# Kernel optimization log

Hardware: AMD Instinct MI355X
Metric: run time of the kernel (lower is better)

## Reference

```python
import jax, jax.numpy as jnp
import numpy as np

NUM_HEADS = 16


def setup_inputs() -> dict:
    key = jax.random.key(0)
    ks = jax.random.split(key, 8)
    B_, N, C = 2048, 64, 512
    nW = 64
    return {
        "x": jax.random.normal(ks[0], (B_, N, C), dtype=jnp.float32),
        "pe": jax.random.normal(ks[1], (1, N, C), dtype=jnp.float32),
        "rpe": jax.random.normal(ks[2], (NUM_HEADS, N, N), dtype=jnp.float32),
        "mask": jax.random.normal(ks[3], (nW, N, N), dtype=jnp.float32),
        "qkv_w": jax.random.normal(ks[4], (3 * C, C), dtype=jnp.float32) * 0.02,
        "qkv_b": jax.random.normal(ks[5], (3 * C,), dtype=jnp.float32) * 0.02,
        "proj_w": jax.random.normal(ks[6], (C, C), dtype=jnp.float32) * 0.02,
        "proj_b": jax.random.normal(ks[7], (C,), dtype=jnp.float32) * 0.02,
    }


def reference(x, pe, rpe, mask, qkv_w, qkv_b, proj_w, proj_b):
    B_, N, C = x.shape
    H = NUM_HEADS
    hd = C // H
    scale = hd ** -0.5
    xp = x + pe  # (B_, N, C)
    qkv = xp @ qkv_w.T + qkv_b  # (B_, N, 3C)
    qkv = qkv.reshape(B_, N, 3, H, hd).transpose(2, 0, 3, 1, 4)  # (3, B_, H, N, hd)
    q, k, v = qkv[0], qkv[1], qkv[2]
    attn = jnp.einsum("bhnd,bhmd->bhnm", q * scale, k)  # (B_, H, N, N)
    attn = attn + rpe[None]  # broadcast rpe over batch
    nW = mask.shape[0]
    attn = attn.reshape(B_ // nW, nW, H, N, N) + mask[None, :, None]
    attn = attn.reshape(B_, H, N, N)
    attn = jax.nn.softmax(attn, axis=-1)
    out = jnp.einsum("bhnm,bhmd->bhnd", attn, v)  # (B_, H, N, hd)
    out = out.transpose(0, 2, 1, 3).reshape(B_, N, C)
    return out @ proj_w.T + proj_b
```

## Files before the change

### kernel.cpp

```cpp
#include <hip/hip_runtime.h>
#include <hip/hip_bf16.h>
#include <cstdint>

typedef __bf16 bf16;
typedef __bf16 bf16x8_t __attribute__((ext_vector_type(8)));
typedef __bf16 bf16x4_t __attribute__((ext_vector_type(4)));
typedef float  f32x4_t  __attribute__((ext_vector_type(4)));

#define MFMA16(a, b, c) __builtin_amdgcn_mfma_f32_16x16x32_bf16((a), (b), (c), 0, 0, 0)

__device__ __forceinline__ void gload_lds16(const bf16* g, bf16* l) {
    __builtin_amdgcn_global_load_lds(
        (const __attribute__((address_space(1))) void*)g,
        (__attribute__((address_space(3))) void*)l,
        16, 0, 0);
}

__global__ void k_wprep(const float* __restrict__ wq, const float* __restrict__ wp,
                        bf16* __restrict__ wqb, bf16* __restrict__ wpb) {
    int t = blockIdx.x * 256 + threadIdx.x;
    int stride = gridDim.x * 256;
    for (int i = t; i < 196608; i += stride) {
        float4 v = ((const float4*)wq)[i];
        bf16x4_t o; o[0]=(bf16)v.x; o[1]=(bf16)v.y; o[2]=(bf16)v.z; o[3]=(bf16)v.w;
        ((bf16x4_t*)wqb)[i] = o;
    }
    for (int i = t; i < 65536; i += stride) {
        float4 v = ((const float4*)wp)[i];
        bf16x4_t o; o[0]=(bf16)v.x; o[1]=(bf16)v.y; o[2]=(bf16)v.z; o[3]=(bf16)v.w;
        ((bf16x4_t*)wpb)[i] = o;
    }
}

__global__ __launch_bounds__(512, 4) void k_qkv_attn(
    const float* __restrict__ x,
    const float* __restrict__ pe,
    const float* __restrict__ rpe,
    const float* __restrict__ mask,
    const float* __restrict__ qkv_b,
    const bf16*  __restrict__ wq,
    bf16* __restrict__ ao)
{
    __shared__ bf16 Ws[96 * 128];
    __shared__ bf16 qs[2][64 * 40];
    __shared__ bf16 ks[2][64 * 40];
    __shared__ bf16 vts[2][32 * 72];
    __shared__ bf16 ps[2][64 * 72];

    const int tid  = threadIdx.x;
    const int lane = tid & 63;
    const int wave = tid >> 6;
    const int win  = wave >> 2;
    const int lr   = lane & 15;
    const int lg   = lane >> 4;
    const int row0 = (wave & 3) * 16;
    const int b2   = blockIdx.x * 2 + win;
    const int wi   = b2 & 63;

    bf16x8_t a[16];
    {
        const float* xr = x  + ((size_t)(b2 * 64 + row0 + lr)) * 512;
        const float* pr = pe + (size_t)(row0 + lr) * 512;
#pragma unroll
        for (int kc = 0; kc < 16; ++kc) {
            int k = kc * 32 + lg * 8;
            float4 x0 = *(const float4*)(xr + k);
            float4 x1 = *(const float4*)(xr + k + 4);
            float4 p0 = *(const float4*)(pr + k);
            float4 p1 = *(const float4*)(pr + k + 4);
            bf16x8_t v;
            v[0]=(bf16)(x0.x+p0.x); v[1]=(bf16)(x0.y+p0.y);
            v[2]=(bf16)(x0.z+p0.z); v[3]=(bf16)(x0.w+p0.w);
            v[4]=(bf16)(x1.x+p1.x); v[5]=(bf16)(x1.y+p1.y);
            v[6]=(bf16)(x1.z+p1.z); v[7]=(bf16)(x1.w+p1.w);
            a[kc] = v;
        }
    }

    const float SCALE = 0.17677669529663687f;

    for (int h = 0; h < 16; ++h) {
        f32x4_t acc[6] = {};
#pragma unroll
        for (int kt = 0; kt < 4; ++kt) {
#pragma unroll
            for (int ii = 0; ii < 3; ++ii) {
                int instr = wave * 3 + ii;
                int r  = instr * 4 + (lane >> 4);
                int s  = lane & 15;
                int gp = (s & 8) | ((s & 7) ^ (r & 7));
                int R  = ((r >> 5) << 9) + (h << 5) + (r & 31);
                gload_lds16(wq + (size_t)R * 512 + kt * 128 + gp * 8,
                            &Ws[instr * 512]);
            }
            __syncthreads();
#pragma unroll
            for (int k2 = 0; k2 < 4; ++k2) {
                const int kc = kt * 4 + k2;
#pragma unroll
                for (int j = 0; j < 6; ++j) {
                    int row  = j * 16 + lr;
                    int p    = k2 * 4 + lg;
                    int phys = (p & 8) | ((p & 7) ^ (row & 7));
                    bf16x8_t bfrag = *(const bf16x8_t*)&Ws[row * 128 + phys * 8];
                    acc[j] = MFMA16(a[kc], bfrag, acc[j]);
                }
            }
            __syncthreads();
        }

#pragma unroll
        for (int j = 0; j < 6; ++j) {
            int which = j >> 1;
            int colh  = (j & 1) * 16 + lr;
            float bj = qkv_b[which * 512 + h * 32 + colh];
#pragma unroll
            for (int r = 0; r < 4; ++r) {
                int row = row0 + lg * 4 + r;
                float val = acc[j][r] + bj;
                if (which == 0)      qs[win][row * 40 + colh] = (bf16)val;
                else if (which == 1) ks[win][row * 40 + colh] = (bf16)val;
                else                 vts[win][colh * 72 + row] = (bf16)val;
            }
        }
        __syncthreads();

        const float* rp = rpe  + ((size_t)h)  * 4096;
        const float* mp = mask + ((size_t)wi) * 4096;
        float rm[4][4];
#pragma unroll
        for (int j = 0; j < 4; ++j) {
            int col = j * 16 + lr;
#pragma unroll
            for (int r = 0; r < 4; ++r) {
                int row = row0 + lg * 4 + r;
                rm[j][r] = rp[row * 64 + col] + mp[row * 64 + col];
            }
        }

        bf16x8_t aq = *(const bf16x8_t*)&qs[win][(row0 + lr) * 40 + lg * 8];
        f32x4_t s[4];
        f32x4_t zero = {};
#pragma unroll
        for (int j = 0; j < 4; ++j) {
            bf16x8_t bk = *(const bf16x8_t*)&ks[win][(j * 16 + lr) * 40 + lg * 8];
            s[j] = MFMA16(aq, bk, zero);
        }

        float mx[4] = {-1e30f, -1e30f, -1e30f, -1e30f};
#pragma unroll
        for (int j = 0; j < 4; ++j)
#pragma unroll
            for (int r = 0; r < 4; ++r) {
                float t = s[j][r] * SCALE + rm[j][r];
                s[j][r] = t;
                mx[r] = fmaxf(mx[r], t);
            }
#pragma unroll
        for (int r = 0; r < 4; ++r) {
            float m = mx[r];
            m = fmaxf(m, __shfl_xor(m, 1));
            m = fmaxf(m, __shfl_xor(m, 2));
            m = fmaxf(m, __shfl_xor(m, 4));
            m = fmaxf(m, __shfl_xor(m, 8));
            mx[r] = m;
        }
        float sm[4] = {0.f, 0.f, 0.f, 0.f};
#pragma unroll
        for (int j = 0; j < 4; ++j)
#pragma unroll
            for (int r = 0; r < 4; ++r) {
                float e = __expf(s[j][r] - mx[r]);
                s[j][r] = e;
                sm[r] += e;
            }
#pragma unroll
        for (int r = 0; r < 4; ++r) {
            float ssum = sm[r];
            ssum += __shfl_xor(ssum, 1);
            ssum += __shfl_xor(ssum, 2);
            ssum += __shfl_xor(ssum, 4);
            ssum += __shfl_xor(ssum, 8);
            sm[r] = 1.0f / ssum;
        }
#pragma unroll
        for (int j = 0; j < 4; ++j)
#pragma unroll
            for (int r = 0; r < 4; ++r)
                ps[win][(row0 + lg * 4 + r) * 72 + j * 16 + lr] = (bf16)s[j][r];

        f32x4_t o[2] = {};
#pragma unroll
        for (int kh = 0; kh < 2; ++kh) {
            bf16x8_t pa = *(const bf16x8_t*)&ps[win][(row0 + lr) * 72 + kh * 32 + lg * 8];
#pragma unroll
            for (int jd = 0; jd < 2; ++jd) {
                bf16x8_t bv = *(const bf16x8_t*)&vts[win][(jd * 16 + lr) * 72 + kh * 32 + lg * 8];
                o[jd] = MFMA16(pa, bv, o[jd]);
            }
        }
#pragma unroll
        for (int jd = 0; jd < 2; ++jd)
#pragma unroll
            for (int r = 0; r < 4; ++r) {
                int row = row0 + lg * 4 + r;
                ao[((size_t)(b2 * 64 + row)) * 512 + h * 32 + jd * 16 + lr] =
                    (bf16)(o[jd][r] * sm[r]);
            }
    }
}

__global__ __launch_bounds__(256) void k_proj(
    const bf16* __restrict__ A, const bf16* __restrict__ Bw,
    const float* __restrict__ bias, float* __restrict__ C)
{
    __shared__ bf16 As[128 * 40];
    __shared__ bf16 Bs[128 * 40];

    const int tid  = threadIdx.x;
    const int lane = tid & 63;
    const int wave = tid >> 6;
    const int lr = lane & 15, lg = lane >> 4;
    const int wr = wave >> 1, wc = wave & 1;
    const int bid = blockIdx.x;
    const int wg  = (bid & 7) * 512 + (bid >> 3);
    const int mb = wg >> 2, nb = wg & 3;
    const size_t m0 = (size_t)mb * 128;
    const int n0 = nb * 128;

    f32x4_t acc[4][4] = {};

    for (int kt = 0; kt < 16; ++kt) {
        const int k0 = kt * 32;
        bf16x8_t va[2], vb[2];
#pragma unroll
        for (int j = 0; j < 2; ++j) {
            int c = tid + 256 * j;
            int row = c >> 2, i8 = (c & 3) * 8;
            va[j] = *(const bf16x8_t*)(A  + (m0 + row) * 512 + k0 + i8);
            vb[j] = *(const bf16x8_t*)(Bw + (size_t)(n0 + row) * 512 + k0 + i8);
        }
        __syncthreads();
#pragma unroll
        for (int j = 0; j < 2; ++j) {
            int c = tid + 256 * j;
            int row = c >> 2, i8 = (c & 3) * 8;
            *(bf16x8_t*)&As[row * 40 + i8] = va[j];
            *(bf16x8_t*)&Bs[row * 40 + i8] = vb[j];
        }
        __syncthreads();

        bf16x8_t af[4], bfr[4];
#pragma unroll
        for (int i = 0; i < 4; ++i)
            af[i] = *(const bf16x8_t*)&As[(wr * 64 + i * 16 + lr) * 40 + lg * 8];
#pragma unroll
        for (int j = 0; j < 4; ++j)
            bfr[j] = *(const bf16x8_t*)&Bs[(wc * 64 + j * 16 + lr) * 40 + lg * 8];
#pragma unroll
        for (int i = 0; i < 4; ++i)
#pragma unroll
            for (int j = 0; j < 4; ++j)
                acc[i][j] = MFMA16(af[i], bfr[j], acc[i][j]);
    }

    float bj[4];
#pragma unroll
    for (int j = 0; j < 4; ++j) bj[j] = bias[n0 + wc * 64 + j * 16 + lr];
#pragma unroll
    for (int i = 0; i < 4; ++i) {
#pragma unroll
        for (int j = 0; j < 4; ++j) {
            int col = n0 + wc * 64 + j * 16 + lr;
#pragma unroll
            for (int r = 0; r < 4; ++r) {
                size_t row = m0 + wr * 64 + i * 16 + lg * 4 + r;
                C[row * 512 + col] = acc[i][j][r] + bj[j];
            }
        }
    }
}

extern "C" void kernel_launch(void* const* d_in, const int* in_sizes, int n_in,
                              void* d_out, int out_size, void* d_ws, size_t ws_size,
                              hipStream_t stream) {
    (void)in_sizes; (void)n_in; (void)out_size; (void)ws_size;
    const float* x      = (const float*)d_in[0];
    const float* pe     = (const float*)d_in[1];
    const float* rpe    = (const float*)d_in[2];
    const float* mask   = (const float*)d_in[3];
    const float* qkv_w  = (const float*)d_in[4];
    const float* qkv_b  = (const float*)d_in[5];
    const float* proj_w = (const float*)d_in[6];
    const float* proj_b = (const float*)d_in[7];
    float* out = (float*)d_out;

    char* ws = (char*)d_ws;
    bf16* wqkvb  = (bf16*)ws;
    bf16* wprojb = (bf16*)(ws + 1572864);
    bf16* ao     = (bf16*)(ws + 2097152);

    k_wprep<<<256, 256, 0, stream>>>(qkv_w, proj_w, wqkvb, wprojb);
    k_qkv_attn<<<1024, 512, 0, stream>>>(x, pe, rpe, mask, qkv_b, wqkvb, ao);
    k_proj<<<4096, 256, 0, stream>>>(ao, wprojb, proj_b, out);
}
```

Before: 762.1 us.

## Double-buffer QKV weight staging and widen proj GEMM K-tile

Double-buffers the per-head QKV weight tile in shared memory so the next tile's global-to-LDS load is issued before computing on the current one. Barriers become explicit waitcnt+s_barrier pairs, and the occupancy hint of 4 blocks per SM is dropped. The projection GEMM now uses a 64-wide K tile with two inner MFMA steps, halving its loop iterations and barriers. Together these add LDS use, which may lower occupancy.

```diff
diff --git a/kernel.cpp b/kernel.cpp
--- a/kernel.cpp
+++ b/kernel.cpp
@@ -32,7 +32,20 @@
     }
 }
 
-__global__ __launch_bounds__(512, 4) void k_qkv_attn(
+__device__ __forceinline__ void stage_ws(const bf16* __restrict__ wq, bf16* wsbuf,
+                                         int h, int kt, int wave, int lane) {
+#pragma unroll
+    for (int ii = 0; ii < 3; ++ii) {
+        int instr = wave * 3 + ii;
+        int rr = instr * 4 + (lane >> 4);
+        int s  = lane & 15;
+        int gp = (s & 8) | ((s & 7) ^ (rr & 7));
+        int R  = ((rr >> 5) << 9) + (h << 5) + (rr & 31);
+        gload_lds16(wq + (size_t)R * 512 + kt * 128 + gp * 8, wsbuf + instr * 512);
+    }
+}
+
+__global__ __launch_bounds__(512) void k_qkv_attn(
     const float* __restrict__ x,
     const float* __restrict__ pe,
     const float* __restrict__ rpe,
@@ -41,7 +54,7 @@
     const bf16*  __restrict__ wq,
     bf16* __restrict__ ao)
 {
-    __shared__ bf16 Ws[96 * 128];
+    __shared__ bf16 Ws[2][96 * 128];
     __shared__ bf16 qs[2][64 * 40];
     __shared__ bf16 ks[2][64 * 40];
     __shared__ bf16 vts[2][32 * 72];
@@ -79,21 +92,21 @@
 
     const float SCALE = 0.17677669529663687f;
 
+    stage_ws(wq, Ws[0], 0, 0, wave, lane);
+
     for (int h = 0; h < 16; ++h) {
         f32x4_t acc[6] = {};
 #pragma unroll
         for (int kt = 0; kt < 4; ++kt) {
-#pragma unroll
-            for (int ii = 0; ii < 3; ++ii) {
-                int instr = wave * 3 + ii;
-                int r  = instr * 4 + (lane >> 4);
-                int s  = lane & 15;
-                int gp = (s & 8) | ((s & 7) ^ (r & 7));
-                int R  = ((r >> 5) << 9) + (h << 5) + (r & 31);
-                gload_lds16(wq + (size_t)R * 512 + kt * 128 + gp * 8,
-                            &Ws[instr * 512]);
-            }
-            __syncthreads();
+            const int ph = h * 4 + kt;
+            if (ph < 63) {
+                const int pn = ph + 1;
+                stage_ws(wq, Ws[(kt + 1) & 1], pn >> 2, pn & 3, wave, lane);
+                asm volatile("s_waitcnt vmcnt(3)" ::: "memory");
+            } else {
+                asm volatile("s_waitcnt vmcnt(0)" ::: "memory");
+            }
+            __builtin_amdgcn_s_barrier();
 #pragma unroll
             for (int k2 = 0; k2 < 4; ++k2) {
                 const int kc = kt * 4 + k2;
@@ -102,11 +115,12 @@
                     int row  = j * 16 + lr;
                     int p    = k2 * 4 + lg;
                     int phys = (p & 8) | ((p & 7) ^ (row & 7));
-                    bf16x8_t bfrag = *(const bf16x8_t*)&Ws[row * 128 + phys * 8];
+                    bf16x8_t bfrag = *(const bf16x8_t*)&Ws[kt & 1][row * 128 + phys * 8];
                     acc[j] = MFMA16(a[kc], bfrag, acc[j]);
                 }
             }
-            __syncthreads();
+            asm volatile("s_waitcnt lgkmcnt(0)" ::: "memory");
+            __builtin_amdgcn_s_barrier();
         }
 
 #pragma unroll
@@ -123,7 +137,8 @@
                 else                 vts[win][colh * 72 + row] = (bf16)val;
             }
         }
-        __syncthreads();
+        asm volatile("s_waitcnt lgkmcnt(0)" ::: "memory");
+        __builtin_amdgcn_s_barrier();
 
         const float* rp = rpe  + ((size_t)h)  * 4096;
         const float* mp = mask + ((size_t)wi) * 4096;
@@ -214,8 +229,8 @@
     const bf16* __restrict__ A, const bf16* __restrict__ Bw,
     const float* __restrict__ bias, float* __restrict__ C)
 {
-    __shared__ bf16 As[128 * 40];
-    __shared__ bf16 Bs[128 * 40];
+    __shared__ bf16 As[128 * 72];
+    __shared__ bf16 Bs[128 * 72];
 
     const int tid  = threadIdx.x;
     const int lane = tid & 63;
@@ -230,38 +245,41 @@
 
     f32x4_t acc[4][4] = {};
 
-    for (int kt = 0; kt < 16; ++kt) {
-        const int k0 = kt * 32;
-        bf16x8_t va[2], vb[2];
-#pragma unroll
-        for (int j = 0; j < 2; ++j) {
+    for (int kt = 0; kt < 8; ++kt) {
+        const int k0 = kt * 64;
+        bf16x8_t va[4], vb[4];
+#pragma unroll
+        for (int j = 0; j < 4; ++j) {
             int c = tid + 256 * j;
-            int row = c >> 2, i8 = (c & 3) * 8;
+            int row = c >> 3, i8 = (c & 7) * 8;
             va[j] = *(const bf16x8_t*)(A  + (m0 + row) * 512 + k0 + i8);
             vb[j] = *(const bf16x8_t*)(Bw + (size_t)(n0 + row) * 512 + k0 + i8);
         }
         __syncthreads();
 #pragma unroll
-        for (int j = 0; j < 2; ++j) {
+        for (int j = 0; j < 4; ++j) {
             int c = tid + 256 * j;
-            int row = c >> 2, i8 = (c & 3) * 8;
-            *(bf16x8_t*)&As[row * 40 + i8] = va[j];
-            *(bf16x8_t*)&Bs[row * 40 + i8] = vb[j];
+            int row = c >> 3, i8 = (c & 7) * 8;
+            *(bf16x8_t*)&As[row * 72 + i8] = va[j];
+            *(bf16x8_t*)&Bs[row * 72 + i8] = vb[j];
         }
         __syncthreads();
 
-        bf16x8_t af[4], bfr[4];
-#pragma unroll
-        for (int i = 0; i < 4; ++i)
-            af[i] = *(const bf16x8_t*)&As[(wr * 64 + i * 16 + lr) * 40 + lg * 8];
-#pragma unroll
-        for (int j = 0; j < 4; ++j)
-            bfr[j] = *(const bf16x8_t*)&Bs[(wc * 64 + j * 16 + lr) * 40 + lg * 8];
-#pragma unroll
-        for (int i = 0; i < 4; ++i)
+#pragma unroll
+        for (int k2 = 0; k2 < 2; ++k2) {
+            bf16x8_t af[4], bfr[4];
+#pragma unroll
+            for (int i = 0; i < 4; ++i)
+                af[i] = *(const bf16x8_t*)&As[(wr * 64 + i * 16 + lr) * 72 + k2 * 32 + lg * 8];
 #pragma unroll
             for (int j = 0; j < 4; ++j)
-                acc[i][j] = MFMA16(af[i], bfr[j], acc[i][j]);
+                bfr[j] = *(const bf16x8_t*)&Bs[(wc * 64 + j * 16 + lr) * 72 + k2 * 32 + lg * 8];
+#pragma unroll
+            for (int i = 0; i < 4; ++i)
+#pragma unroll
+                for (int j = 0; j < 4; ++j)
+                    acc[i][j] = MFMA16(af[i], bfr[j], acc[i][j]);
+        }
     }
 
     float bj[4];
```

Result: faster. 675.1 us (-11.4%).
